# Kernel optimization log

Measured on AMD Instinct MI355X. Metric: run time of the kernel, lower is better.

## Reference

```python
import jax, jax.numpy as jnp
import numpy as np

D = 40       # d_model
SL = 10      # sequenceLength
AN = 268     # actionNum
B = 8192     # batch


def relu6(x):
    return jnp.clip(x, 0.0, 6.0)


def setup_inputs() -> dict:
    key = jax.random.key(0)
    ks = jax.random.split(key, 16)
    s = 1.0 / np.sqrt(D)
    X = jax.random.randint(ks[0], (B, SL, 4), 0, AN)
    t1 = jax.random.randint(ks[1], (B, SL - 1), 0, 7)
    t2 = jax.random.randint(ks[2], (B, SL - 1), 0, 8)
    # per-step Linear(1, D): weight [D,1] -> store as [SL-1, D]; kaiming-uniform bound 1/sqrt(1)=1
    Ew = jax.random.uniform(ks[3], (SL - 1, D), minval=-1.0, maxval=1.0)
    Eb = jax.random.uniform(ks[4], (SL - 1, D), minval=-1.0, maxval=1.0)
    Qw = jax.random.uniform(ks[5], (SL - 1, D, D), minval=-s, maxval=s)
    Qb = jax.random.uniform(ks[6], (SL - 1, D), minval=-s, maxval=s)
    Lw = jax.random.uniform(ks[7], (SL - 1, D * D, D), minval=-s, maxval=s)
    Lb = jax.random.uniform(ks[8], (SL - 1, D * D), minval=-s, maxval=s)
    Mw = jax.random.uniform(ks[9], (SL - 1, D, D), minval=-s, maxval=s)
    Mb = jax.random.uniform(ks[10], (SL - 1, D), minval=-s, maxval=s)
    Tw = jax.random.uniform(ks[11], (AN, D), minval=-s, maxval=s)
    Tb = jax.random.uniform(ks[12], (AN,), minval=-s, maxval=s)
    emb = jax.random.normal(ks[13], (AN, D))
    return dict(X=X, t1=t1, t2=t2, Ew=Ew, Eb=Eb, Qw=Qw, Qb=Qb, Lw=Lw, Lb=Lb,
                Mw=Mw, Mb=Mb, Tw=Tw, Tb=Tb, emb=emb)


def reference(X, t1, t2, Ew, Eb, Qw, Qb, Lw, Lb, Mw, Mb, Tw, Tb, emb):
    b = X.shape[0]
    t = (t1 * 8 + t2).astype(jnp.float32)          # [B, SL-1]
    ae = emb[X[:, :SL - 1, 3]]                     # [B, SL-1, D]

    def step(carry, xs):
        h0, p0 = carry
        ew, eb, qw, qb, lw, lb, mw, mb, ti, ei = xs
        # E(t_i) + Q(p0), both [B, D]
        p1 = relu6(ti[:, None] * ew[None, :] + eb + p0 @ qw.T + qb)
        # hypernetwork-generated per-sample matrix [B, D, D]
        jt = relu6(p1 @ lw.T + lb).reshape(b, D, D)
        tt = jnp.einsum('bd,bde->be', h0, jt)
        h1 = relu6(ei @ mw.T + mb + tt)
        return (h1, p1), None

    xs = (Ew, Eb, Qw, Qb, Lw, Lb, Mw, Mb, t.T, jnp.swapaxes(ae, 0, 1))
    init = (jnp.zeros((b, D), jnp.float32), jnp.zeros((b, D), jnp.float32))
    (h0, _), _ = jax.lax.scan(step, init, xs)
    return h0 @ Tw.T + Tb                          # [B, AN]
```

## Files before the change

### kernel.cpp

```cpp
#include <hip/hip_runtime.h>

#define DD 40
#define SLM1 9
#define ANUM 268
#define MB 32

typedef __attribute__((ext_vector_type(8))) short short8;
typedef __attribute__((ext_vector_type(4))) float f32x4;
typedef __attribute__((ext_vector_type(16))) float f32x16;

#define WS_LWF ((size_t)0)
#define WS_LWT ((size_t)552960)
#define WS_QW  ((size_t)691200)
#define WS_MW  ((size_t)718848)
#define WS_TW  ((size_t)746496)

__device__ __forceinline__ unsigned short f2bf(float f){
  unsigned int u = __float_as_uint(f);
  u += 0x7FFFu + ((u >> 16) & 1u);
  return (unsigned short)(u >> 16);
}
__device__ __forceinline__ float relu6f(float v){
  return fminf(fmaxf(v, 0.0f), 6.0f);
}

__device__ __forceinline__ f32x16 mfma3(short8 a0, short8 a1, short8 a2,
                                        short8 b0, short8 b1, short8 b2){
  f32x16 c = {0,0,0,0,0,0,0,0,0,0,0,0,0,0,0,0};
  c = __builtin_amdgcn_mfma_f32_32x32x16_bf16(a0, b0, c, 0, 0, 0);
  c = __builtin_amdgcn_mfma_f32_32x32x16_bf16(a1, b1, c, 0, 0, 0);
  c = __builtin_amdgcn_mfma_f32_32x32x16_bf16(a2, b2, c, 0, 0, 0);
  return c;
}

__global__ __launch_bounds__(256)
void prep_frags(const float* __restrict__ Qw, const float* __restrict__ Lw,
                const float* __restrict__ Mw, const float* __restrict__ Tw,
                const float* __restrict__ Ew, const float* __restrict__ Eb,
                const float* __restrict__ Qb, const float* __restrict__ Lb,
                const float* __restrict__ Mb, const float* __restrict__ Tb,
                unsigned short* __restrict__ ws)
{
  const int bid = blockIdx.x, tid = threadIdx.x;
  if (bid < 360){
    int s = bid / 40, d = bid - s*40;
    unsigned short* dst = ws + WS_LWF + (size_t)bid*1536;
    const float* W = Lw + (size_t)s*64000;
    const float* bv = Lb + (size_t)s*1600;
    for (int i = tid; i < 1536; i += 256){
      int kf = i >> 9, q = i & 511, l = q >> 3, j = q & 7;
      int k = kf*16 + ((l >> 5) << 3) + j;
      int e = l & 31;
      int n = d*DD + e;
      float v = 0.f;
      if (k < DD) v = W[n*DD + k];
      else if (k == DD) v = bv[n];
      dst[i] = f2bf(v);
    }
  } else if (bid < 450){
    int t = bid - 360;
    int s = t / 10, tt = t - s*10;
    unsigned short* dst = ws + WS_LWT + (size_t)t*1536;
    const float* W = Lw + (size_t)s*64000;
    const float* bv = Lb + (size_t)s*1600;
    for (int i = tid; i < 1536; i += 256){
      int kf = i >> 9, q = i & 511, l = q >> 3, j = q & 7;
      int k = kf*16 + ((l >> 5) << 3) + j;
      int c = l & 31;
      int d = 4*tt + (c >> 3);
      int e = 32 + (c & 7);
      int n = d*DD + e;
      float v = 0.f;
      if (k < DD) v = W[n*DD + k];
      else if (k == DD) v = bv[n];
      dst[i] = f2bf(v);
    }
  } else if (bid < 459){
    int s = bid - 450;
    unsigned short* dst = ws + WS_QW + (size_t)s*3072;
    const float* W = Qw + (size_t)s*1600;
    for (int i = tid; i < 3072; i += 256){
      int et = i / 1536, r = i - et*1536;
      int kf = r >> 9, q = r & 511, l = q >> 3, j = q & 7;
      int k = kf*16 + ((l >> 5) << 3) + j;
      int jc = et*32 + (l & 31);
      float v = 0.f;
      if (jc < DD){
        if (k < DD) v = W[jc*DD + k];
        else if (k == DD) v = Eb[s*DD + jc] + Qb[s*DD + jc];
        else if (k == DD+1) v = Ew[s*DD + jc];
      }
      dst[i] = f2bf(v);
    }
  } else if (bid < 468){
    int s = bid - 459;
    unsigned short* dst = ws + WS_MW + (size_t)s*3072;
    const float* W = Mw + (size_t)s*1600;
    for (int i = tid; i < 3072; i += 256){
      int et = i / 1536, r = i - et*1536;
      int kf = r >> 9, q = r & 511, l = q >> 3, j = q & 7;
      int k = kf*16 + ((l >> 5) << 3) + j;
      int e = et*32 + (l & 31);
      float v = 0.f;
      if (e < DD){
        if (k < DD) v = W[e*DD + k];
        else if (k == DD) v = Mb[s*DD + e];
      }
      dst[i] = f2bf(v);
    }
  } else {
    int t = bid - 468;
    unsigned short* dst = ws + WS_TW + (size_t)t*1536;
    for (int i = tid; i < 1536; i += 256){
      int kf = i >> 9, q = i & 511, l = q >> 3, j = q & 7;
      int k = kf*16 + ((l >> 5) << 3) + j;
      int a = t*32 + (l & 31);
      float v = 0.f;
      if (a < ANUM){
        if (k < DD) v = Tw[(size_t)a*DD + k];
        else if (k == DD) v = Tb[a];
      }
      dst[i] = f2bf(v);
    }
  }
}

__global__ __launch_bounds__(512)
void star_main(const int* __restrict__ X,
               const int* __restrict__ T1,
               const int* __restrict__ T2,
               const float* __restrict__ emb,
               const unsigned short* __restrict__ ws,
               float* __restrict__ out)
{
  __shared__ __align__(16) unsigned short pbuf[2][3072];
  __shared__ __align__(16) unsigned short aebf[2][3072];
  __shared__ __align__(16) float hT[2][DD*36];
  __shared__ __align__(16) float red[8][MB*DD];
  __shared__ int   aeidx[SLM1][MB];
  __shared__ float tvtab[SLM1][MB];

  const int tid = threadIdx.x;
  const int w = __builtin_amdgcn_readfirstlane(tid >> 6);
  const int l = tid & 63;
  const int col = l & 31, half = l >> 5;
  const int row0 = blockIdx.x * MB;

  {
    unsigned int* p = (unsigned int*)&pbuf[0][0];
    for (int i = tid; i < 3072; i += 512) p[i] = 0u;
    unsigned int* a = (unsigned int*)&aebf[0][0];
    for (int i = tid; i < 3072; i += 512) a[i] = 0u;
    float* rr = &red[0][0];
    for (int i = tid; i < 8*MB*DD; i += 512) rr[i] = 0.f;
  }
  if (tid < MB*SLM1){
    int m = tid / SLM1, s = tid - m*SLM1;
    int r = row0 + m;
    aeidx[s][m] = X[(size_t)r*40 + s*4 + 3];
    tvtab[s][m] = (float)(T1[r*SLM1 + s]*8 + T2[r*SLM1 + s]);
  }
  __syncthreads();
  if (tid < MB){
    int off = 2*1024 + (tid + 32)*8;
    pbuf[0][off] = 0x3F80; pbuf[1][off] = 0x3F80;
    aebf[0][off] = 0x3F80; aebf[1][off] = 0x3F80;
    pbuf[0][off+1] = f2bf(tvtab[0][tid]);
    pbuf[1][off+1] = f2bf(tvtab[1][tid]);
  }
  if (tid < 320){
    int m = tid / 10, q4 = tid - m*10;
    float4 v4 = *(const float4*)(emb + (size_t)aeidx[0][m]*DD + q4*4);
    #pragma unroll
    for (int c2 = 0; c2 < 4; ++c2){
      int k = q4*4 + c2, kf = k >> 4, kk = k & 15;
      aebf[0][kf*1024 + (m + ((kk >> 3) << 5))*8 + (kk & 7)] = f2bf(((const float*)&v4)[c2]);
    }
  }
  __syncthreads();
  if (w < 2){
    short8 a0 = ((const short8*)&pbuf[0][0])[l];
    short8 a1 = ((const short8*)&pbuf[0][1024])[l];
    short8 a2 = ((const short8*)&pbuf[0][2048])[l];
    const unsigned short* qwb = ws + WS_QW + w*1536;
    f32x16 c = mfma3(a0, a1, a2, ((const short8*)qwb)[l],
                     ((const short8*)(qwb+512))[l], ((const short8*)(qwb+1024))[l]);
    int j = w*32 + col;
    if (j < DD){
      int kf = j >> 4, kk = j & 15;
      #pragma unroll
      for (int r = 0; r < 16; ++r){
        int m = (r & 3) + ((r >> 2) << 3) + (half << 2);
        pbuf[1][kf*1024 + (m + ((kk >> 3) << 5))*8 + (kk & 7)] = f2bf(relu6f(c[r]));
      }
    }
  }
  __syncthreads();

  short8 q00, q01, q02, q10, q11, q12;

  for (int s = 0; s < SLM1; ++s){
    const int pcur = (s + 1) & 1;
    const int hrd  = s & 1;

    float4 gv; int gm = 0, gq = 0;
    const bool dog = (s < 8) && (tid < 320);
    if (dog){
      gm = tid / 10; gq = tid - gm*10;
      gv = *(const float4*)(emb + (size_t)aeidx[s+1][gm]*DD + gq*4);
    }
    short8 pa0 = ((const short8*)&pbuf[pcur][0])[l];
    short8 pa1 = ((const short8*)&pbuf[pcur][1024])[l];
    short8 pa2 = ((const short8*)&pbuf[pcur][2048])[l];
    if (s > 0){
      const float* hbase = &hT[hrd][half << 2];

      f32x16 tt = {0,0,0,0,0,0,0,0,0,0,0,0,0,0,0,0};
      {
        const unsigned short* lwf = ws + WS_LWF + (size_t)(s*40)*1536;
        short8 b00 = q00, b01 = q01, b02 = q02;
        short8 b10 = q10, b11 = q11, b12 = q12;
        #pragma unroll
        for (int i = 0; i < 5; ++i){
          short8 nb0, nb1, nb2;
          if (i < 3){
            const unsigned short* nf = lwf + (size_t)((i+2)*8 + w)*1536;
            nb0 = ((const short8*)nf)[l];
            nb1 = ((const short8*)(nf + 512))[l];
            nb2 = ((const short8*)(nf + 1024))[l];
          }
          const float* hb = hbase + (i*8 + w)*36;
          f32x4 h0 = *(const f32x4*)(hb);
          f32x4 h1 = *(const f32x4*)(hb + 8);
          f32x4 h2 = *(const f32x4*)(hb + 16);
          f32x4 h3 = *(const f32x4*)(hb + 24);
          f32x16 c = mfma3(pa0, pa1, pa2, b00, b01, b02);
          #pragma unroll
          for (int q = 0; q < 4; ++q){
            tt[q]    = fmaf(h0[q], relu6f(c[q]),    tt[q]);
            tt[4+q]  = fmaf(h1[q], relu6f(c[4+q]),  tt[4+q]);
            tt[8+q]  = fmaf(h2[q], relu6f(c[8+q]),  tt[8+q]);
            tt[12+q] = fmaf(h3[q], relu6f(c[12+q]), tt[12+q]);
          }
          b00 = b10; b01 = b11; b02 = b12;
          if (i < 3){ b10 = nb0; b11 = nb1; b12 = nb2; }
        }
      }
      #pragma unroll
      for (int r = 0; r < 16; ++r){
        int m = (r & 3) + ((r >> 2) << 3) + (half << 2);
        red[w][m*DD + col] = tt[r];
      }
    }

    if (s < 8){
      const unsigned short* nl = ws + WS_LWF + (size_t)((s+1)*40)*1536;
      const unsigned short* n0 = nl + (size_t)w*1536;
      q00 = ((const short8*)n0)[l];
      q01 = ((const short8*)(n0 + 512))[l];
      q02 = ((const short8*)(n0 + 1024))[l];
      const unsigned short* n1 = nl + (size_t)(8 + w)*1536;
      q10 = ((const short8*)n1)[l];
      q11 = ((const short8*)(n1 + 512))[l];
      q12 = ((const short8*)(n1 + 1024))[l];
    }

    if (s > 0 && w < 6){
      const unsigned short* lwt = ws + WS_LWT + (size_t)(s*10)*1536;
      f32x16 tacc = {0,0,0,0,0,0,0,0,0,0,0,0,0,0,0,0};
      for (int tti = w; tti < 10; tti += 6){
        const unsigned short* ft = lwt + (size_t)tti*1536;
        short8 t0 = ((const short8*)ft)[l];
        short8 t1 = ((const short8*)(ft + 512))[l];
        short8 t2 = ((const short8*)(ft + 1024))[l];
        f32x16 c = mfma3(pa0, pa1, pa2, t0, t1, t2);
        int dt = 4*tti + (col >> 3);
        const float* hb = &hT[hrd][dt*36 + (half << 2)];
        #pragma unroll
        for (int g = 0; g < 4; ++g){
          f32x4 hg = *(const f32x4*)(hb + g*8);
          #pragma unroll
          for (int q = 0; q < 4; ++q){
            float val = hg[q]*relu6f(c[g*4+q]);
            val += __shfl_xor(val, 8);
            val += __shfl_xor(val, 16);
            tacc[g*4+q] += val;
          }
        }
      }
      if (col < 8){
        #pragma unroll
        for (int r = 0; r < 16; ++r){
          int m = (r & 3) + ((r >> 2) << 3) + (half << 2);
          red[w][m*DD + 32 + col] = tacc[r];
        }
      }
    } else if (w >= 6 && s < 8){
      const int et = w - 6;
      const unsigned short* qwb = ws + WS_QW + (size_t)(s+1)*3072 + (size_t)et*1536;
      f32x16 c = mfma3(pa0, pa1, pa2, ((const short8*)qwb)[l],
                       ((const short8*)(qwb+512))[l], ((const short8*)(qwb+1024))[l]);
      int j = et*32 + col;
      if (j < DD){
        int kf = j >> 4, kk = j & 15;
        #pragma unroll
        for (int r = 0; r < 16; ++r){
          int m = (r & 3) + ((r >> 2) << 3) + (half << 2);
          pbuf[s & 1][kf*1024 + (m + ((kk >> 3) << 5))*8 + (kk & 7)] = f2bf(relu6f(c[r]));
        }
      }
    }
    if (dog){
      unsigned short* dst = &aebf[(s+1) & 1][0];
      #pragma unroll
      for (int c2 = 0; c2 < 4; ++c2){
        int k = gq*4 + c2, kf = k >> 4, kk = k & 15;
        dst[kf*1024 + (gm + ((kk >> 3) << 5))*8 + (kk & 7)] = f2bf(((const float*)&gv)[c2]);
      }
    }
    if (s <= 6 && tid < MB)
      pbuf[s & 1][2*1024 + (tid + 32)*8 + 1] = f2bf(tvtab[s+2][tid]);
    __syncthreads();

    if (w < 2){
      short8 a0 = ((const short8*)&aebf[s & 1][0])[l];
      short8 a1 = ((const short8*)&aebf[s & 1][1024])[l];
      short8 a2 = ((const short8*)&aebf[s & 1][2048])[l];
      const unsigned short* mwb = ws + WS_MW + (size_t)s*3072 + w*1536;
      int e = w*32 + col;
      f32x16 c = {0,0,0,0,0,0,0,0,0,0,0,0,0,0,0,0};
      if (e < DD){
        #pragma unroll
        for (int r = 0; r < 16; ++r){
          int m = (r & 3) + ((r >> 2) << 3) + (half << 2);
          float acc = red[0][m*DD + e];
          #pragma unroll
          for (int dp = 1; dp < 8; ++dp) acc += red[dp][m*DD + e];
          c[r] = acc;
        }
      }
      c = __builtin_amdgcn_mfma_f32_32x32x16_bf16(a0, ((const short8*)mwb)[l], c, 0, 0, 0);
      c = __builtin_amdgcn_mfma_f32_32x32x16_bf16(a1, ((const short8*)(mwb+512))[l], c, 0, 0, 0);
      c = __builtin_amdgcn_mfma_f32_32x32x16_bf16(a2, ((const short8*)(mwb+1024))[l], c, 0, 0, 0);
      if (e < DD){
        int kf = e >> 4, kk = e & 15;
        #pragma unroll
        for (int r = 0; r < 16; ++r){
          int m = (r & 3) + ((r >> 2) << 3) + (half << 2);
          float v = relu6f(c[r]);
          hT[(s+1) & 1][e*36 + m] = v;
          if (s == SLM1-1)
            aebf[1][kf*1024 + (m + ((kk >> 3) << 5))*8 + (kk & 7)] = f2bf(v);
        }
      }
    }
    __syncthreads();
  }

  for (int t = w; t < 9; t += 8){
    short8 a0 = ((const short8*)&aebf[1][0])[l];
    short8 a1 = ((const short8*)&aebf[1][1024])[l];
    short8 a2 = ((const short8*)&aebf[1][2048])[l];
    const unsigned short* twb = ws + WS_TW + (size_t)t*1536;
    f32x16 c = mfma3(a0, a1, a2, ((const short8*)twb)[l],
                     ((const short8*)(twb+512))[l], ((const short8*)(twb+1024))[l]);
    int a = t*32 + col;
    if (a < ANUM){
      #pragma unroll
      for (int r = 0; r < 16; ++r){
        int m = (r & 3) + ((r >> 2) << 3) + (half << 2);
        out[(size_t)(row0 + m)*ANUM + a] = c[r];
      }
    }
  }
}

extern "C" void kernel_launch(void* const* d_in, const int* in_sizes, int n_in,
                              void* d_out, int out_size, void* d_ws, size_t ws_size,
                              hipStream_t stream) {
  const int*   X  = (const int*)  d_in[0];
  const int*   T1 = (const int*)  d_in[1];
  const int*   T2 = (const int*)  d_in[2];
  const float* Ew = (const float*)d_in[3];
  const float* Eb = (const float*)d_in[4];
  const float* Qw = (const float*)d_in[5];
  const float* Qb = (const float*)d_in[6];
  const float* Lw = (const float*)d_in[7];
  const float* Lb = (const float*)d_in[8];
  const float* Mw = (const float*)d_in[9];
  const float* Mb = (const float*)d_in[10];
  const float* Tw = (const float*)d_in[11];
  const float* Tb = (const float*)d_in[12];
  const float* em = (const float*)d_in[13];
  unsigned short* ws = (unsigned short*)d_ws;
  float* out = (float*)d_out;

  prep_frags<<<dim3(477), dim3(256), 0, stream>>>(Qw, Lw, Mw, Tw, Ew, Eb, Qb,
                                                  Lb, Mb, Tb, ws);
  star_main<<<dim3(8192 / MB), dim3(512), 0, stream>>>(X, T1, T2, em, ws, out);
}
```

Before: 57.32 us.

## Widen block to 12 waves and rebalance hypernetwork tiles across waves

Raises the block from 8 to 12 waves. Ten waves each handle four of the forty LWF tiles plus one LWT tile, and two waves compute the next Q projection. The partial-sum buffer is re-laid out interleaved (12 slots per output element) so the final reduction reads three float4 vectors instead of eight strided scalars. The goal is to spread the per-step matrix work across more waves and balance load. The cost is more register pressure under the 768-thread launch bound and a larger shared-memory footprint, which may reduce occupancy.

```diff
diff --git a/kernel.cpp b/kernel.cpp
--- a/kernel.cpp
+++ b/kernel.cpp
@@ -125,7 +125,7 @@
   }
 }
 
-__global__ __launch_bounds__(512)
+__global__ __launch_bounds__(768)
 void star_main(const int* __restrict__ X,
                const int* __restrict__ T1,
                const int* __restrict__ T2,
@@ -136,7 +136,7 @@
   __shared__ __align__(16) unsigned short pbuf[2][3072];
   __shared__ __align__(16) unsigned short aebf[2][3072];
   __shared__ __align__(16) float hT[2][DD*36];
-  __shared__ __align__(16) float red[8][MB*DD];
+  __shared__ __align__(16) float red[MB*DD*12];
   __shared__ int   aeidx[SLM1][MB];
   __shared__ float tvtab[SLM1][MB];
 
@@ -148,11 +148,10 @@
 
   {
     unsigned int* p = (unsigned int*)&pbuf[0][0];
-    for (int i = tid; i < 3072; i += 512) p[i] = 0u;
+    for (int i = tid; i < 3072; i += 768) p[i] = 0u;
     unsigned int* a = (unsigned int*)&aebf[0][0];
-    for (int i = tid; i < 3072; i += 512) a[i] = 0u;
-    float* rr = &red[0][0];
-    for (int i = tid; i < 8*MB*DD; i += 512) rr[i] = 0.f;
+    for (int i = tid; i < 3072; i += 768) a[i] = 0u;
+    for (int i = tid; i < MB*DD*12; i += 768) red[i] = 0.f;
   }
   if (tid < MB*SLM1){
     int m = tid / SLM1, s = tid - m*SLM1;
@@ -197,7 +196,7 @@
   }
   __syncthreads();
 
-  short8 q00, q01, q02, q10, q11, q12;
+  short8 q00, q01, q02;
 
   for (int s = 0; s < SLM1; ++s){
     const int pcur = (s + 1) & 1;
@@ -212,70 +211,54 @@
     short8 pa0 = ((const short8*)&pbuf[pcur][0])[l];
     short8 pa1 = ((const short8*)&pbuf[pcur][1024])[l];
     short8 pa2 = ((const short8*)&pbuf[pcur][2048])[l];
-    if (s > 0){
+
+    if (s > 0 && w < 10){
       const float* hbase = &hT[hrd][half << 2];
+      const unsigned short* lwf = ws + WS_LWF + (size_t)(s*40)*1536;
 
       f32x16 tt = {0,0,0,0,0,0,0,0,0,0,0,0,0,0,0,0};
-      {
-        const unsigned short* lwf = ws + WS_LWF + (size_t)(s*40)*1536;
-        short8 b00 = q00, b01 = q01, b02 = q02;
-        short8 b10 = q10, b11 = q11, b12 = q12;
-        #pragma unroll
-        for (int i = 0; i < 5; ++i){
-          short8 nb0, nb1, nb2;
-          if (i < 3){
-            const unsigned short* nf = lwf + (size_t)((i+2)*8 + w)*1536;
-            nb0 = ((const short8*)nf)[l];
-            nb1 = ((const short8*)(nf + 512))[l];
-            nb2 = ((const short8*)(nf + 1024))[l];
-          }
-          const float* hb = hbase + (i*8 + w)*36;
-          f32x4 h0 = *(const f32x4*)(hb);
-          f32x4 h1 = *(const f32x4*)(hb + 8);
-          f32x4 h2 = *(const f32x4*)(hb + 16);
-          f32x4 h3 = *(const f32x4*)(hb + 24);
-          f32x16 c = mfma3(pa0, pa1, pa2, b00, b01, b02);
-          #pragma unroll
-          for (int q = 0; q < 4; ++q){
-            tt[q]    = fmaf(h0[q], relu6f(c[q]),    tt[q]);
-            tt[4+q]  = fmaf(h1[q], relu6f(c[4+q]),  tt[4+q]);
-            tt[8+q]  = fmaf(h2[q], relu6f(c[8+q]),  tt[8+q]);
-            tt[12+q] = fmaf(h3[q], relu6f(c[12+q]), tt[12+q]);
-          }
-          b00 = b10; b01 = b11; b02 = b12;
-          if (i < 3){ b10 = nb0; b11 = nb1; b12 = nb2; }
-        }
+      short8 b0 = q00, b1 = q01, b2 = q02;
+      #pragma unroll
+      for (int i = 0; i < 4; ++i){
+        const unsigned short* nf = (i < 3)
+            ? lwf + (size_t)((i+1)*10 + w)*1536
+            : ws + WS_LWT + (size_t)(s*10 + w)*1536;
+        short8 n0 = ((const short8*)nf)[l];
+        short8 n1 = ((const short8*)(nf + 512))[l];
+        short8 n2 = ((const short8*)(nf + 1024))[l];
+        const float* hb = hbase + (i*10 + w)*36;
+        f32x4 h0 = *(const f32x4*)(hb);
+        f32x4 h1 = *(const f32x4*)(hb + 8);
+        f32x4 h2 = *(const f32x4*)(hb + 16);
+        f32x4 h3 = *(const f32x4*)(hb + 24);
+        f32x16 c = mfma3(pa0, pa1, pa2, b0, b1, b2);
+        #pragma unroll
+        for (int q = 0; q < 4; ++q){
+          tt[q]    = fmaf(h0[q], relu6f(c[q]),    tt[q]);
+          tt[4+q]  = fmaf(h1[q], relu6f(c[4+q]),  tt[4+q]);
+          tt[8+q]  = fmaf(h2[q], relu6f(c[8+q]),  tt[8+q]);
+          tt[12+q] = fmaf(h3[q], relu6f(c[12+q]), tt[12+q]);
+        }
+        b0 = n0; b1 = n1; b2 = n2;
       }
       #pragma unroll
       for (int r = 0; r < 16; ++r){
         int m = (r & 3) + ((r >> 2) << 3) + (half << 2);
-        red[w][m*DD + col] = tt[r];
-      }
-    }
-
-    if (s < 8){
-      const unsigned short* nl = ws + WS_LWF + (size_t)((s+1)*40)*1536;
-      const unsigned short* n0 = nl + (size_t)w*1536;
-      q00 = ((const short8*)n0)[l];
-      q01 = ((const short8*)(n0 + 512))[l];
-      q02 = ((const short8*)(n0 + 1024))[l];
-      const unsigned short* n1 = nl + (size_t)(8 + w)*1536;
-      q10 = ((const short8*)n1)[l];
-      q11 = ((const short8*)(n1 + 512))[l];
-      q12 = ((const short8*)(n1 + 1024))[l];
-    }
-
-    if (s > 0 && w < 6){
-      const unsigned short* lwt = ws + WS_LWT + (size_t)(s*10)*1536;
-      f32x16 tacc = {0,0,0,0,0,0,0,0,0,0,0,0,0,0,0,0};
-      for (int tti = w; tti < 10; tti += 6){
-        const unsigned short* ft = lwt + (size_t)tti*1536;
-        short8 t0 = ((const short8*)ft)[l];
-        short8 t1 = ((const short8*)(ft + 512))[l];
-        short8 t2 = ((const short8*)(ft + 1024))[l];
-        f32x16 c = mfma3(pa0, pa1, pa2, t0, t1, t2);
-        int dt = 4*tti + (col >> 3);
+        red[(m*DD + col)*12 + w] = tt[r];
+      }
+
+      if (s < 8){
+        const unsigned short* n0p = ws + WS_LWF + (size_t)((s+1)*40 + w)*1536;
+        q00 = ((const short8*)n0p)[l];
+        q01 = ((const short8*)(n0p + 512))[l];
+        q02 = ((const short8*)(n0p + 1024))[l];
+      }
+
+      {
+        f32x16 c = mfma3(pa0, pa1, pa2, b0, b1, b2);
+        int dt = 4*w + (col >> 3);
         const float* hb = &hT[hrd][dt*36 + (half << 2)];
+        f32x16 tacc;
         #pragma unroll
         for (int g = 0; g < 4; ++g){
           f32x4 hg = *(const f32x4*)(hb + g*8);
@@ -284,19 +267,24 @@
             float val = hg[q]*relu6f(c[g*4+q]);
             val += __shfl_xor(val, 8);
             val += __shfl_xor(val, 16);
-            tacc[g*4+q] += val;
+            tacc[g*4+q] = val;
           }
         }
-      }
-      if (col < 8){
-        #pragma unroll
-        for (int r = 0; r < 16; ++r){
-          int m = (r & 3) + ((r >> 2) << 3) + (half << 2);
-          red[w][m*DD + 32 + col] = tacc[r];
-        }
-      }
-    } else if (w >= 6 && s < 8){
-      const int et = w - 6;
+        if (col < 8){
+          #pragma unroll
+          for (int r = 0; r < 16; ++r){
+            int m = (r & 3) + ((r >> 2) << 3) + (half << 2);
+            red[(m*DD + 32 + col)*12 + w] = tacc[r];
+          }
+        }
+      }
+    } else if (s == 0 && w < 10 && s < 8){
+      const unsigned short* n0p = ws + WS_LWF + (size_t)((s+1)*40 + w)*1536;
+      q00 = ((const short8*)n0p)[l];
+      q01 = ((const short8*)(n0p + 512))[l];
+      q02 = ((const short8*)(n0p + 1024))[l];
+    } else if (w >= 10 && s < 8){
+      const int et = w - 10;
       const unsigned short* qwb = ws + WS_QW + (size_t)(s+1)*3072 + (size_t)et*1536;
       f32x16 c = mfma3(pa0, pa1, pa2, ((const short8*)qwb)[l],
                        ((const short8*)(qwb+512))[l], ((const short8*)(qwb+1024))[l]);
@@ -333,10 +321,11 @@
         #pragma unroll
         for (int r = 0; r < 16; ++r){
           int m = (r & 3) + ((r >> 2) << 3) + (half << 2);
-          float acc = red[0][m*DD + e];
-          #pragma unroll
-          for (int dp = 1; dp < 8; ++dp) acc += red[dp][m*DD + e];
-          c[r] = acc;
+          const f32x4* rp = (const f32x4*)&red[(m*DD + e)*12];
+          f32x4 v0 = rp[0], v1 = rp[1], v2 = rp[2];
+          c[r] = ((v0[0]+v0[1])+(v0[2]+v0[3]))
+               + ((v1[0]+v1[1])+(v1[2]+v1[3]))
+               + ((v2[0]+v2[1])+(v2[2]+v2[3]));
         }
       }
       c = __builtin_amdgcn_mfma_f32_32x32x16_bf16(a0, ((const short8*)mwb)[l], c, 0, 0, 0);
@@ -357,7 +346,8 @@
     __syncthreads();
   }
 
-  for (int t = w; t < 9; t += 8){
+  if (w < 9){
+    const int t = w;
     short8 a0 = ((const short8*)&aebf[1][0])[l];
     short8 a1 = ((const short8*)&aebf[1][1024])[l];
     short8 a2 = ((const short8*)&aebf[1][2048])[l];
@@ -397,5 +387,5 @@
 
   prep_frags<<<dim3(477), dim3(256), 0, stream>>>(Qw, Lw, Mw, Tw, Ew, Eb, Qb,
                                                   Lb, Mb, Tb, ws);
-  star_main<<<dim3(8192 / MB), dim3(512), 0, stream>>>(X, T1, T2, em, ws, out);
-}
+  star_main<<<dim3(8192 / MB), dim3(768), 0, stream>>>(X, T1, T2, em, ws, out);
+}
```

Result: slower. 69.82 us (+21.8%).

## Interleave paired MFMA chains and prefetch LWT/QW fragments in hypernet loop

Applied to the files above, without the earlier changes.

Restructures the per-step hypernetwork loop so each wave processes two d-tiles at once with interleaved MFMA accumulation chains, giving the matrix unit independent work between dependent MFMAs. The last iteration also prefetches the LWT or QW fragment that the following tail or Q-projection stage needs, hiding its global load latency behind the main MFMA work. The prep kernel is also launched with 512 threads per block. The cost is higher register pressure from the extra live fragments and accumulators.

```diff
diff --git a/kernel.cpp b/kernel.cpp
--- a/kernel.cpp
+++ b/kernel.cpp
@@ -33,7 +33,7 @@
   return c;
 }
 
-__global__ __launch_bounds__(256)
+__global__ __launch_bounds__(512)
 void prep_frags(const float* __restrict__ Qw, const float* __restrict__ Lw,
                 const float* __restrict__ Mw, const float* __restrict__ Tw,
                 const float* __restrict__ Ew, const float* __restrict__ Eb,
@@ -47,7 +47,7 @@
     unsigned short* dst = ws + WS_LWF + (size_t)bid*1536;
     const float* W = Lw + (size_t)s*64000;
     const float* bv = Lb + (size_t)s*1600;
-    for (int i = tid; i < 1536; i += 256){
+    for (int i = tid; i < 1536; i += 512){
       int kf = i >> 9, q = i & 511, l = q >> 3, j = q & 7;
       int k = kf*16 + ((l >> 5) << 3) + j;
       int e = l & 31;
@@ -63,7 +63,7 @@
     unsigned short* dst = ws + WS_LWT + (size_t)t*1536;
     const float* W = Lw + (size_t)s*64000;
     const float* bv = Lb + (size_t)s*1600;
-    for (int i = tid; i < 1536; i += 256){
+    for (int i = tid; i < 1536; i += 512){
       int kf = i >> 9, q = i & 511, l = q >> 3, j = q & 7;
       int k = kf*16 + ((l >> 5) << 3) + j;
       int c = l & 31;
@@ -79,7 +79,7 @@
     int s = bid - 450;
     unsigned short* dst = ws + WS_QW + (size_t)s*3072;
     const float* W = Qw + (size_t)s*1600;
-    for (int i = tid; i < 3072; i += 256){
+    for (int i = tid; i < 3072; i += 512){
       int et = i / 1536, r = i - et*1536;
       int kf = r >> 9, q = r & 511, l = q >> 3, j = q & 7;
       int k = kf*16 + ((l >> 5) << 3) + j;
@@ -96,7 +96,7 @@
     int s = bid - 459;
     unsigned short* dst = ws + WS_MW + (size_t)s*3072;
     const float* W = Mw + (size_t)s*1600;
-    for (int i = tid; i < 3072; i += 256){
+    for (int i = tid; i < 3072; i += 512){
       int et = i / 1536, r = i - et*1536;
       int kf = r >> 9, q = r & 511, l = q >> 3, j = q & 7;
       int k = kf*16 + ((l >> 5) << 3) + j;
@@ -111,7 +111,7 @@
   } else {
     int t = bid - 468;
     unsigned short* dst = ws + WS_TW + (size_t)t*1536;
-    for (int i = tid; i < 1536; i += 256){
+    for (int i = tid; i < 1536; i += 512){
       int kf = i >> 9, q = i & 511, l = q >> 3, j = q & 7;
       int k = kf*16 + ((l >> 5) << 3) + j;
       int a = t*32 + (l & 31);
@@ -212,38 +212,75 @@
     short8 pa0 = ((const short8*)&pbuf[pcur][0])[l];
     short8 pa1 = ((const short8*)&pbuf[pcur][1024])[l];
     short8 pa2 = ((const short8*)&pbuf[pcur][2048])[l];
+
+    short8 A0, A1, A2, B0, B1, B2;
+
     if (s > 0){
       const float* hbase = &hT[hrd][half << 2];
-
+      const unsigned short* lwf = ws + WS_LWF + (size_t)(s*40)*1536;
+
+      A0 = q00; A1 = q01; A2 = q02;
+      B0 = q10; B1 = q11; B2 = q12;
       f32x16 tt = {0,0,0,0,0,0,0,0,0,0,0,0,0,0,0,0};
-      {
-        const unsigned short* lwf = ws + WS_LWF + (size_t)(s*40)*1536;
-        short8 b00 = q00, b01 = q01, b02 = q02;
-        short8 b10 = q10, b11 = q11, b12 = q12;
-        #pragma unroll
-        for (int i = 0; i < 5; ++i){
-          short8 nb0, nb1, nb2;
-          if (i < 3){
-            const unsigned short* nf = lwf + (size_t)((i+2)*8 + w)*1536;
-            nb0 = ((const short8*)nf)[l];
-            nb1 = ((const short8*)(nf + 512))[l];
-            nb2 = ((const short8*)(nf + 1024))[l];
-          }
-          const float* hb = hbase + (i*8 + w)*36;
-          f32x4 h0 = *(const f32x4*)(hb);
-          f32x4 h1 = *(const f32x4*)(hb + 8);
-          f32x4 h2 = *(const f32x4*)(hb + 16);
-          f32x4 h3 = *(const f32x4*)(hb + 24);
-          f32x16 c = mfma3(pa0, pa1, pa2, b00, b01, b02);
+
+      #pragma unroll
+      for (int it = 0; it < 2; ++it){
+        short8 NA0, NA1, NA2, NB0, NB1, NB2;
+        if (it == 0){
+          const unsigned short* fA = lwf + (size_t)(16 + w)*1536;
+          NA0 = ((const short8*)fA)[l];
+          NA1 = ((const short8*)(fA + 512))[l];
+          NA2 = ((const short8*)(fA + 1024))[l];
+          const unsigned short* fB = lwf + (size_t)(24 + w)*1536;
+          NB0 = ((const short8*)fB)[l];
+          NB1 = ((const short8*)(fB + 512))[l];
+          NB2 = ((const short8*)(fB + 1024))[l];
+        } else {
+          const unsigned short* fA = lwf + (size_t)(32 + w)*1536;
+          NA0 = ((const short8*)fA)[l];
+          NA1 = ((const short8*)(fA + 512))[l];
+          NA2 = ((const short8*)(fA + 1024))[l];
+          const size_t qs = (s < 8) ? (size_t)(s + 1) : (size_t)8;
+          const unsigned short* fB = (w < 6)
+              ? ws + WS_LWT + (size_t)(s*10 + w)*1536
+              : ws + WS_QW + qs*3072 + (size_t)(w - 6)*1536;
+          NB0 = ((const short8*)fB)[l];
+          NB1 = ((const short8*)(fB + 512))[l];
+          NB2 = ((const short8*)(fB + 1024))[l];
+        }
+        f32x16 ca = {0,0,0,0,0,0,0,0,0,0,0,0,0,0,0,0};
+        f32x16 cb = {0,0,0,0,0,0,0,0,0,0,0,0,0,0,0,0};
+        ca = __builtin_amdgcn_mfma_f32_32x32x16_bf16(pa0, A0, ca, 0, 0, 0);
+        cb = __builtin_amdgcn_mfma_f32_32x32x16_bf16(pa0, B0, cb, 0, 0, 0);
+        ca = __builtin_amdgcn_mfma_f32_32x32x16_bf16(pa1, A1, ca, 0, 0, 0);
+        cb = __builtin_amdgcn_mfma_f32_32x32x16_bf16(pa1, B1, cb, 0, 0, 0);
+        ca = __builtin_amdgcn_mfma_f32_32x32x16_bf16(pa2, A2, ca, 0, 0, 0);
+        cb = __builtin_amdgcn_mfma_f32_32x32x16_bf16(pa2, B2, cb, 0, 0, 0);
+        const int dA = it*16 + w, dB = it*16 + 8 + w;
+        const float* hA = hbase + dA*36;
+        const float* hB = hbase + dB*36;
+        #pragma unroll
+        for (int g = 0; g < 4; ++g){
+          f32x4 ha = *(const f32x4*)(hA + g*8);
+          f32x4 hb = *(const f32x4*)(hB + g*8);
           #pragma unroll
           for (int q = 0; q < 4; ++q){
-            tt[q]    = fmaf(h0[q], relu6f(c[q]),    tt[q]);
-            tt[4+q]  = fmaf(h1[q], relu6f(c[4+q]),  tt[4+q]);
-            tt[8+q]  = fmaf(h2[q], relu6f(c[8+q]),  tt[8+q]);
-            tt[12+q] = fmaf(h3[q], relu6f(c[12+q]), tt[12+q]);
+            tt[g*4+q] = fmaf(ha[q], relu6f(ca[g*4+q]), tt[g*4+q]);
+            tt[g*4+q] = fmaf(hb[q], relu6f(cb[g*4+q]), tt[g*4+q]);
           }
-          b00 = b10; b01 = b11; b02 = b12;
-          if (i < 3){ b10 = nb0; b11 = nb1; b12 = nb2; }
+        }
+        A0 = NA0; A1 = NA1; A2 = NA2;
+        B0 = NB0; B1 = NB1; B2 = NB2;
+      }
+      {
+        f32x16 c = mfma3(pa0, pa1, pa2, A0, A1, A2);
+        const float* hb = hbase + (32 + w)*36;
+        #pragma unroll
+        for (int g = 0; g < 4; ++g){
+          f32x4 hg = *(const f32x4*)(hb + g*8);
+          #pragma unroll
+          for (int q = 0; q < 4; ++q)
+            tt[g*4+q] = fmaf(hg[q], relu6f(c[g*4+q]), tt[g*4+q]);
         }
       }
       #pragma unroll
@@ -267,14 +304,32 @@
 
     if (s > 0 && w < 6){
       const unsigned short* lwt = ws + WS_LWT + (size_t)(s*10)*1536;
+      const float* hb0;
       f32x16 tacc = {0,0,0,0,0,0,0,0,0,0,0,0,0,0,0,0};
-      for (int tti = w; tti < 10; tti += 6){
-        const unsigned short* ft = lwt + (size_t)tti*1536;
+      {
+        f32x16 c = mfma3(pa0, pa1, pa2, B0, B1, B2);
+        int dt = 4*w + (col >> 3);
+        hb0 = &hT[hrd][dt*36 + (half << 2)];
+        #pragma unroll
+        for (int g = 0; g < 4; ++g){
+          f32x4 hg = *(const f32x4*)(hb0 + g*8);
+          #pragma unroll
+          for (int q = 0; q < 4; ++q){
+            float val = hg[q]*relu6f(c[g*4+q]);
+            val += __shfl_xor(val, 8);
+            val += __shfl_xor(val, 16);
+            tacc[g*4+q] += val;
+          }
+        }
+      }
+      if (w < 4){
+        const int t2 = w + 6;
+        const unsigned short* ft = lwt + (size_t)t2*1536;
         short8 t0 = ((const short8*)ft)[l];
         short8 t1 = ((const short8*)(ft + 512))[l];
-        short8 t2 = ((const short8*)(ft + 1024))[l];
-        f32x16 c = mfma3(pa0, pa1, pa2, t0, t1, t2);
-        int dt = 4*tti + (col >> 3);
+        short8 t2r = ((const short8*)(ft + 1024))[l];
+        f32x16 c = mfma3(pa0, pa1, pa2, t0, t1, t2r);
+        int dt = 4*t2 + (col >> 3);
         const float* hb = &hT[hrd][dt*36 + (half << 2)];
         #pragma unroll
         for (int g = 0; g < 4; ++g){
@@ -296,11 +351,17 @@
         }
       }
     } else if (w >= 6 && s < 8){
-      const int et = w - 6;
-      const unsigned short* qwb = ws + WS_QW + (size_t)(s+1)*3072 + (size_t)et*1536;
-      f32x16 c = mfma3(pa0, pa1, pa2, ((const short8*)qwb)[l],
-                       ((const short8*)(qwb+512))[l], ((const short8*)(qwb+1024))[l]);
-      int j = et*32 + col;
+      short8 Q0, Q1, Q2;
+      if (s == 0){
+        const unsigned short* qwb = ws + WS_QW + (size_t)(s+1)*3072 + (size_t)(w-6)*1536;
+        Q0 = ((const short8*)qwb)[l];
+        Q1 = ((const short8*)(qwb + 512))[l];
+        Q2 = ((const short8*)(qwb + 1024))[l];
+      } else {
+        Q0 = B0; Q1 = B1; Q2 = B2;
+      }
+      f32x16 c = mfma3(pa0, pa1, pa2, Q0, Q1, Q2);
+      int j = (w - 6)*32 + col;
       if (j < DD){
         int kf = j >> 4, kk = j & 15;
         #pragma unroll
@@ -395,7 +456,7 @@
   unsigned short* ws = (unsigned short*)d_ws;
   float* out = (float*)d_out;
 
-  prep_frags<<<dim3(477), dim3(256), 0, stream>>>(Qw, Lw, Mw, Tw, Ew, Eb, Qb,
+  prep_frags<<<dim3(477), dim3(512), 0, stream>>>(Qw, Lw, Mw, Tw, Ew, Eb, Qb,
                                                   Lb, Mb, Tb, ws);
   star_main<<<dim3(8192 / MB), dim3(512), 0, stream>>>(X, T1, T2, em, ws, out);
 }
```

Measured after the change: 55.53 us. -3.1%, faster.
